# Kernel optimization log

Measured on AMD Instinct MI355X. Metric: run time of the kernel, lower is better.

The kernel has to match this reference:

```python
import jax, jax.numpy as jnp
import numpy as np

NT = 100000   # total word nodes (B graphs * N nodes)
B = 50        # number of graphs in the batch
E = 1600000   # total edges
V = 15000     # vocab (num_word)
D_IN = 128    # h_inp
D_H = 128     # h_dim


def setup_inputs() -> dict:
    key = jax.random.key(0)
    ks = jax.random.split(key, 12)
    return {
        "node_ids": jax.random.randint(ks[0], (NT,), 0, V),
        "src": jax.random.randint(ks[1], (E,), 0, NT),
        "dst": jax.random.randint(ks[2], (E,), 0, NT),
        "edge_weight": jax.random.uniform(ks[3], (E,), dtype=jnp.float32),
        "y_data": jax.random.uniform(ks[4], (B,), dtype=jnp.float32),
        "word_embeds": jax.random.normal(ks[5], (V, D_IN), dtype=jnp.float32) * 0.1,
        "W1": jax.random.normal(ks[6], (D_IN, D_H), dtype=jnp.float32) * 0.05,
        "b1": jax.random.normal(ks[7], (D_H,), dtype=jnp.float32) * 0.05,
        "W2": jax.random.normal(ks[8], (D_H, D_H), dtype=jnp.float32) * 0.05,
        "b2": jax.random.normal(ks[9], (D_H,), dtype=jnp.float32) * 0.05,
        "W_out": jax.random.normal(ks[10], (D_H, 1), dtype=jnp.float32) * 0.05,
        "b_out": jax.random.normal(ks[11], (1,), dtype=jnp.float32) * 0.05,
    }


def _word_graph_layer(h, W, b, src, dst, edge_weight, deg):
    # Linear projection, then DGL u_mul_e + mean aggregation over incoming edges.
    Wh = h @ W + b                                   # [NT, D]
    m = Wh[src] * edge_weight[:, None]               # gather + edge-weight mul, [E, D]
    s = jax.ops.segment_sum(m, dst, num_segments=NT)  # scatter-add, [NT, D]
    # mean over incoming messages; nodes with no in-edges keep 0 (DGL semantics)
    return jnp.where(deg[:, None] > 0, s / jnp.maximum(deg, 1.0)[:, None], 0.0)


def reference(node_ids, src, dst, edge_weight, y_data, word_embeds,
              W1, b1, W2, b2, W_out, b_out):
    deg = jax.ops.segment_sum(jnp.ones_like(edge_weight), dst, num_segments=NT)
    h = word_embeds[node_ids]                        # [NT, D_IN]
    h = _word_graph_layer(h, W1, b1, src, dst, edge_weight, deg)
    h = jax.nn.leaky_relu(h, negative_slope=0.01)
    h = _word_graph_layer(h, W2, b2, src, dst, edge_weight, deg)
    # per-graph mean pool; equal graph sizes so padded mean == true mean
    word_pool = h.reshape(B, NT // B, D_H).mean(axis=1)   # [B, D_H]
    logits = (word_pool @ W_out + b_out).reshape(-1)      # [B]
    # binary_cross_entropy_with_logits, mean reduction (numerically stable)
    loss = jnp.mean(jnp.maximum(logits, 0.0) - logits * y_data
                    + jnp.log1p(jnp.exp(-jnp.abs(logits))))
    y_pred = jax.nn.sigmoid(logits)[:, None]              # [B, 1]
    return (loss, y_pred)
```

## Files before the change

### kernel.cpp

```cpp
#include <hip/hip_runtime.h>
#include <hip/hip_fp16.h>
#include <math.h>

#define NT 100000
#define B_GRAPHS 50
#define NE 1600000
#define V 15000
#define D 128
#define NODES_PER_GRAPH (NT / B_GRAPHS)

#define POOL_N (B_GRAPHS * D + B_GRAPHS)

#define BSH 8
#define BIN_DSTS 256
#define NBIN ((NT + BIN_DSTS - 1) / BIN_DSTS)
#define SLACK (3 * BIN_DSTS)
#define EPB 4096
#define NFB ((NE + EPB - 1) / EPB)
#define BUF_SORT 5632
#define PAY_CAP2 (NE + NBIN * SLACK + 256)

__device__ __forceinline__ unsigned enc2_e5m2(float a, float b) {
  unsigned ha = __half_as_ushort(__float2half(a));
  unsigned hb = __half_as_ushort(__float2half(b));
  ha = ((ha + 0x7fu + ((ha >> 8) & 1u)) >> 8) & 0xffu;
  hb = ((hb + 0x7fu + ((hb >> 8) & 1u)) >> 8) & 0xffu;
  return ha | (hb << 8);
}
__device__ __forceinline__ unsigned enc4_e5m2(float a, float b, float c, float d) {
  return enc2_e5m2(a, b) | (enc2_e5m2(c, d) << 16);
}
__device__ __forceinline__ float4 dec4_e5m2(unsigned u) {
  unsigned hp0 = ((u & 0xffu) << 8) | ((u & 0xff00u) << 16);
  unsigned hp1 = ((u >> 8) & 0xff00u) | (u & 0xff000000u);
  __half2 h0 = *(__half2*)&hp0;
  __half2 h1 = *(__half2*)&hp1;
  float2 f0 = __half22float2(h0);
  float2 f1 = __half22float2(h1);
  return make_float4(f0.x, f0.y, f1.x, f1.y);
}

#define PR 16
__global__ __launch_bounds__(256, 8)
void k_project(const float* __restrict__ embeds,
               const float* __restrict__ W1,
               const float* __restrict__ b1,
               unsigned* __restrict__ P1p8) {
  __shared__ float sE[PR][D];
  __shared__ float sO[PR][D];
  int t = threadIdx.x;
  int row0 = blockIdx.x * PR;
  for (int i = t; i < PR * D; i += 256) {
    int r = i >> 7, c = i & 127;
    int v = row0 + r;
    sE[r][c] = (v < V) ? embeds[(size_t)v * D + c] : 0.f;
  }
  __syncthreads();
  int c = t & 127, rg = (t >> 7) * 8;
  float bd = b1[c];
  float acc[8];
#pragma unroll
  for (int r = 0; r < 8; ++r) acc[r] = bd;
#pragma unroll 4
  for (int k = 0; k < D; ++k) {
    float w = W1[k * D + c];
#pragma unroll
    for (int r = 0; r < 8; ++r) acc[r] = fmaf(sE[rg + r][k], w, acc[r]);
  }
#pragma unroll
  for (int r = 0; r < 8; ++r) sO[rg + r][c] = acc[r];
  __syncthreads();
  for (int i = t; i < PR * 32; i += 256) {
    int r = i >> 5, li = i & 31;
    int v = row0 + r;
    if (v < V)
      P1p8[(size_t)v * 32 + li] =
          enc4_e5m2(sO[r][4 * li], sO[r][4 * li + 1], sO[r][4 * li + 2], sO[r][4 * li + 3]);
  }
}

__global__ __launch_bounds__(512)
void k_hist(const int* __restrict__ dst, int* __restrict__ binCnt) {
  __shared__ int h[NBIN];
  int t = threadIdx.x;
  for (int i = t; i < NBIN; i += 512) h[i] = 0;
  __syncthreads();
  int base = blockIdx.x * EPB;
#pragma unroll
  for (int i = 0; i < EPB / 512; ++i) {
    int e = base + i * 512 + t;
    if (e < NE) atomicAdd(&h[dst[e] >> BSH], 1);
  }
  __syncthreads();
  for (int i = t; i < NBIN; i += 512)
    if (h[i]) atomicAdd(&binCnt[i], h[i]);
}

__global__ void k_binscan(const int* __restrict__ binCnt,
                          int* __restrict__ stageBase, int* __restrict__ payBase) {
  __shared__ int s[512], p[512];
  int t = threadIdx.x;
  int c = (t < NBIN) ? binCnt[t] : 0;
  int cp = (t < NBIN) ? (c + SLACK) : 0;
  s[t] = c; p[t] = cp;
  __syncthreads();
  for (int off = 1; off < 512; off <<= 1) {
    int a = (t >= off) ? s[t - off] : 0;
    int b = (t >= off) ? p[t - off] : 0;
    __syncthreads();
    s[t] += a; p[t] += b;
    __syncthreads();
  }
  if (t < NBIN) { stageBase[t] = s[t] - c; payBase[t] = p[t] - cp; }
}

__global__ __launch_bounds__(512)
void k_binfill(const int* __restrict__ src, const int* __restrict__ dst,
               const float* __restrict__ ew, const int* __restrict__ node_ids,
               const int* __restrict__ stageBase, int* __restrict__ binCursor,
               int2* __restrict__ stage) {
  __shared__ int h[512], sc[512], gbase[512], cur[512];
  __shared__ int2 buf[EPB];
  int t = threadIdx.x;
  h[t] = 0;
  __syncthreads();
  int base = blockIdx.x * EPB;
  int d_[EPB / 512], b_[EPB / 512];
#pragma unroll
  for (int i = 0; i < EPB / 512; ++i) {
    int e = base + i * 512 + t;
    int d = (e < NE) ? dst[e] : -1;
    d_[i] = d;
    b_[i] = (d >= 0) ? (d >> BSH) : -1;
    if (d >= 0) atomicAdd(&h[b_[i]], 1);
  }
  __syncthreads();
  int c = h[t];
  sc[t] = c;
  __syncthreads();
  for (int off = 1; off < 512; off <<= 1) {
    int a = (t >= off) ? sc[t - off] : 0;
    __syncthreads();
    sc[t] += a;
    __syncthreads();
  }
  cur[t] = sc[t] - c;
  if (t < NBIN && c > 0) gbase[t] = atomicAdd(&binCursor[t], c);
  __syncthreads();
#pragma unroll
  for (int i = 0; i < EPB / 512; ++i) {
    int e = base + i * 512 + t;
    if (e < NE) {
      int s = src[e];
      unsigned uw = __float_as_uint(ew[e]);
      unsigned wb = (uw + 0x7fffu + ((uw >> 16) & 1u)) & 0xffff0000u;
      int wid = node_ids[s];
      int dl = d_[i] & (BIN_DSTS - 1);
      int p = atomicAdd(&cur[b_[i]], 1);
      buf[p] = make_int2((int)(wb | (unsigned)wid), s | (dl << 17));
    }
  }
  __syncthreads();
  for (int b = t; b < NBIN; b += 512) {
    int len = h[b];
    if (!len) continue;
    int gp = stageBase[b] + gbase[b];
    int lp = sc[b] - len;
    for (int k = 0; k < len; ++k) stage[gp + k] = buf[lp + k];
  }
}

__global__ __launch_bounds__(256)
void k_binsort(const int2* __restrict__ stage, const int* __restrict__ binCnt,
               const int* __restrict__ stageBase, const int* __restrict__ payBase,
               int* __restrict__ rowD, int* __restrict__ cntD,
               int2* __restrict__ pay) {
  __shared__ int h2[BIN_DSTS], ro[BIN_DSTS], cur2[BIN_DSTS];
  __shared__ int2 buf[BUF_SORT];
  int b = blockIdx.x, t = threadIdx.x;
  int cnt = binCnt[b], sb = stageBase[b], pb = payBase[b];
  int dst0 = b << BSH;
  h2[t] = 0;
  __syncthreads();
  for (int i = t; i < cnt; i += 256)
    atomicAdd(&h2[(stage[sb + i].y >> 17) & 255], 1);
  __syncthreads();
  int c = h2[t];
  int pc = (c + 3) & ~3;
  ro[t] = pc;
  __syncthreads();
  for (int off = 1; off < 256; off <<= 1) {
    int a = (t >= off) ? ro[t - off] : 0;
    __syncthreads();
    ro[t] += a;
    __syncthreads();
  }
  int myoff = ro[t] - pc;
  int n = dst0 + t;
  if (n < NT) { rowD[n] = pb + myoff; cntD[n] = c; }
  cur2[t] = myoff;
  __syncthreads();
  int ztot = cnt + SLACK;
  for (int i = t; i < ztot; i += 256) buf[i] = make_int2(0, 0);
  __syncthreads();
  for (int i = t; i < cnt; i += 256) {
    int2 r = stage[sb + i];
    int dl = (r.y >> 17) & 255;
    int p = atomicAdd(&cur2[dl], 1);
    buf[p] = make_int2(r.x, r.y & 0x1ffff);
  }
  __syncthreads();
  for (int i = t; i < ztot; i += 256) pay[pb + i] = buf[i];
}

template<bool USE_WID>
__device__ __forceinline__ int pick_idx(const int4& q, int half) {
  int lo = USE_WID ? (q.x & 0xffff) : q.y;
  int hi = USE_WID ? (q.z & 0xffff) : q.w;
  return half ? hi : lo;
}
__device__ __forceinline__ void consume2(const int4& q, unsigned v, int half,
                                         float& a0, float& a1, float& a2, float& a3,
                                         float& sw) {
  int wm = half ? q.z : q.x;
  float w = __uint_as_float((unsigned)wm & 0xffff0000u);
  float4 x = dec4_e5m2(v);
  a0 = fmaf(w, x.x, a0); a1 = fmaf(w, x.y, a1);
  a2 = fmaf(w, x.z, a2); a3 = fmaf(w, x.w, a3);
  sw += w;
}

template<bool USE_WID>
__device__ __forceinline__ void gather_row(const int2* __restrict__ pay,
                                           const unsigned* __restrict__ tab,
                                           int beg, int cnt, int li, int half,
                                           float& a0, float& a1, float& a2, float& a3,
                                           float& sw) {
  int G = (cnt + 3) >> 2;
  const int4* __restrict__ pp = (const int4*)(pay + beg);
  int4 q0a = pp[0], q0b = pp[1];
  int4 q1a = pp[2], q1b = pp[3];
  int4 q2a = pp[4], q2b = pp[5];
  int4 q3a = pp[6], q3b = pp[7];
  int4 q4a = pp[8], q4b = pp[9];
  unsigned va0 = tab[(size_t)pick_idx<USE_WID>(q0a, half) * 32 + li];
  unsigned vb0 = tab[(size_t)pick_idx<USE_WID>(q0b, half) * 32 + li];
  unsigned va1 = tab[(size_t)pick_idx<USE_WID>(q1a, half) * 32 + li];
  unsigned vb1 = tab[(size_t)pick_idx<USE_WID>(q1b, half) * 32 + li];
  unsigned va2 = tab[(size_t)pick_idx<USE_WID>(q2a, half) * 32 + li];
  unsigned vb2 = tab[(size_t)pick_idx<USE_WID>(q2b, half) * 32 + li];
  for (int g = 0; g < G; ++g) {
    unsigned vn0 = tab[(size_t)pick_idx<USE_WID>(q3a, half) * 32 + li];
    unsigned vn1 = tab[(size_t)pick_idx<USE_WID>(q3b, half) * 32 + li];
    int4 qna = pp[2 * g + 10];
    int4 qnb = pp[2 * g + 11];
    consume2(q0a, va0, half, a0, a1, a2, a3, sw);
    consume2(q0b, vb0, half, a0, a1, a2, a3, sw);
    q0a = q1a; q0b = q1b; q1a = q2a; q1b = q2b; q2a = q3a; q2b = q3b;
    q3a = q4a; q3b = q4b; q4a = qna; q4b = qnb;
    va0 = va1; vb0 = vb1; va1 = va2; vb1 = vb2; va2 = vn0; vb2 = vn1;
  }
}

__global__ void k_agg1(const int2* __restrict__ pay,
                       const int* __restrict__ rowD, const int* __restrict__ cntD,
                       const unsigned* __restrict__ P1p8,
                       unsigned* __restrict__ h1p8) {
  int n = blockIdx.x * 4 + (threadIdx.x >> 6);
  int lane = threadIdx.x & 63;
  int li = lane & 31, half = lane >> 5;
  int beg = __builtin_amdgcn_readfirstlane(rowD[n]);
  int cnt = __builtin_amdgcn_readfirstlane(cntD[n]);
  float a0 = 0.f, a1 = 0.f, a2 = 0.f, a3 = 0.f, sw = 0.f;
  gather_row<true>(pay, P1p8, beg, cnt, li, half, a0, a1, a2, a3, sw);
  a0 += __shfl_down(a0, 32);
  a1 += __shfl_down(a1, 32);
  a2 += __shfl_down(a2, 32);
  a3 += __shfl_down(a3, 32);
  if (lane < 32) {
    float inv = (cnt > 0) ? (1.0f / (float)cnt) : 0.0f;
    float x0 = a0 * inv, x1 = a1 * inv, x2 = a2 * inv, x3 = a3 * inv;
    x0 = (x0 > 0.f) ? x0 : 0.01f * x0;
    x1 = (x1 > 0.f) ? x1 : 0.01f * x1;
    x2 = (x2 > 0.f) ? x2 : 0.01f * x2;
    x3 = (x3 > 0.f) ? x3 : 0.01f * x3;
    h1p8[(size_t)n * 32 + li] = enc4_e5m2(x0, x1, x2, x3);
  }
}

#define NPW2 10
#define BLKS_PER_G (NODES_PER_GRAPH / (4 * NPW2))
__global__ void k_agg2(const int2* __restrict__ pay,
                       const int* __restrict__ rowD, const int* __restrict__ cntD,
                       const unsigned* __restrict__ h1p8,
                       float* __restrict__ pool) {
  int g = blockIdx.x / BLKS_PER_G;
  int chunk = blockIdx.x % BLKS_PER_G;
  int w = threadIdx.x >> 6, lane = threadIdx.x & 63;
  int li = lane & 31, half = lane >> 5;
  int nbase = g * NODES_PER_GRAPH + chunk * (4 * NPW2) + w * NPW2;
  float s0 = 0.f, s1 = 0.f, s2 = 0.f, s3 = 0.f, sc = 0.f;
  for (int i = 0; i < NPW2; ++i) {
    int n = nbase + i;
    int beg = __builtin_amdgcn_readfirstlane(rowD[n]);
    int cnt = __builtin_amdgcn_readfirstlane(cntD[n]);
    float a0 = 0.f, a1 = 0.f, a2 = 0.f, a3 = 0.f, sw = 0.f;
    gather_row<false>(pay, h1p8, beg, cnt, li, half, a0, a1, a2, a3, sw);
    float inv = (cnt > 0) ? (1.0f / (float)cnt) : 0.0f;
    s0 = fmaf(a0, inv, s0); s1 = fmaf(a1, inv, s1);
    s2 = fmaf(a2, inv, s2); s3 = fmaf(a3, inv, s3);
    sc = fmaf(sw, inv, sc);
  }
  s0 += __shfl_down(s0, 32);
  s1 += __shfl_down(s1, 32);
  s2 += __shfl_down(s2, 32);
  s3 += __shfl_down(s3, 32);
  sc += __shfl_down(sc, 32);
  __shared__ float sS[4 * 128];
  __shared__ float sC[4];
  if (lane < 32) {
    sS[w * 128 + 4 * li + 0] = s0;
    sS[w * 128 + 4 * li + 1] = s1;
    sS[w * 128 + 4 * li + 2] = s2;
    sS[w * 128 + 4 * li + 3] = s3;
  }
  if (lane == 0) sC[w] = sc;
  __syncthreads();
  int t = threadIdx.x;
  if (t < 128) {
    float v = sS[t] + sS[128 + t] + sS[256 + t] + sS[384 + t];
    atomicAdd(&pool[g * D + t], v);
  }
  if (t == 0) atomicAdd(&pool[B_GRAPHS * D + g], sC[0] + sC[1] + sC[2] + sC[3]);
}

__global__ void k_final(const float* __restrict__ poolS, const float* __restrict__ poolC,
                        const float* __restrict__ W2, const float* __restrict__ b2,
                        const float* __restrict__ W_out, const float* __restrict__ b_out,
                        const float* __restrict__ y, float* __restrict__ out) {
  int t = threadIdx.x;
  __shared__ float w2o[D];
  __shared__ float red[D];
  __shared__ float s2o_sh;
  __shared__ float logits[B_GRAPHS];
  float acc = 0.f;
  for (int d = 0; d < D; ++d) acc = fmaf(W2[t * D + d], W_out[d], acc);
  w2o[t] = acc;
  red[t] = b2[t] * W_out[t];
  __syncthreads();
  for (int off = 64; off > 0; off >>= 1) {
    if (t < off) red[t] += red[t + off];
    __syncthreads();
  }
  if (t == 0) s2o_sh = red[0];
  __syncthreads();
  float s2o = s2o_sh;
  float bout = b_out[0];
  const float invN = 1.0f / (float)NODES_PER_GRAPH;
  for (int g = 0; g < B_GRAPHS; ++g) {
    red[t] = poolS[g * D + t] * w2o[t];
    __syncthreads();
    for (int off = 64; off > 0; off >>= 1) {
      if (t < off) red[t] += red[t + off];
      __syncthreads();
    }
    if (t == 0) logits[g] = red[0] * invN + poolC[g] * invN * s2o + bout;
    __syncthreads();
  }
  float term = 0.f;
  if (t < B_GRAPHS) {
    float l = logits[t];
    out[1 + t] = 1.0f / (1.0f + expf(-l));
    term = fmaxf(l, 0.f) - l * y[t] + log1pf(expf(-fabsf(l)));
  }
  red[t] = term;
  __syncthreads();
  for (int off = 64; off > 0; off >>= 1) {
    if (t < off) red[t] += red[t + off];
    __syncthreads();
  }
  if (t == 0) out[0] = red[0] / (float)B_GRAPHS;
}

extern "C" void kernel_launch(void* const* d_in, const int* in_sizes, int n_in,
                              void* d_out, int out_size, void* d_ws, size_t ws_size,
                              hipStream_t stream) {
  const int*   node_ids = (const int*)d_in[0];
  const int*   src      = (const int*)d_in[1];
  const int*   dst      = (const int*)d_in[2];
  const float* ew       = (const float*)d_in[3];
  const float* y        = (const float*)d_in[4];
  const float* embeds   = (const float*)d_in[5];
  const float* W1       = (const float*)d_in[6];
  const float* b1       = (const float*)d_in[7];
  const float* W2       = (const float*)d_in[8];
  const float* b2       = (const float*)d_in[9];
  const float* W_out    = (const float*)d_in[10];
  const float* b_out    = (const float*)d_in[11];
  float* out = (float*)d_out;
  (void)in_sizes; (void)n_in; (void)out_size; (void)ws_size;

  char* ws = (char*)d_ws;
  size_t off = 0;
  auto alloc = [&](size_t bytes) {
    size_t r = off;
    off = (off + bytes + 511) & ~(size_t)511;
    return r;
  };
  size_t o_binCnt = alloc(512 * 4);
  size_t o_binCur = alloc(512 * 4);
  size_t o_pool   = alloc((size_t)POOL_N * 4);
  size_t zero_end = off;
  size_t o_sBase  = alloc(512 * 4);
  size_t o_pBase  = alloc(512 * 4);
  size_t o_rowD   = alloc((size_t)NT * 4);
  size_t o_cntD   = alloc((size_t)NT * 4);
  size_t o_P1p8   = alloc((size_t)V * 32 * 4);
  size_t o_h1p8   = alloc((size_t)NT * 32 * 4);
  size_t o_stage  = alloc((size_t)NE * 8);
  size_t o_pay    = alloc((size_t)PAY_CAP2 * 8);

  int*      binCnt   = (int*)(ws + o_binCnt);
  int*      binCursor= (int*)(ws + o_binCur);
  float*    pool     = (float*)(ws + o_pool);
  int*      stageBase= (int*)(ws + o_sBase);
  int*      payBase  = (int*)(ws + o_pBase);
  int*      rowD     = (int*)(ws + o_rowD);
  int*      cntD     = (int*)(ws + o_cntD);
  unsigned* P1p8     = (unsigned*)(ws + o_P1p8);
  unsigned* h1p8     = (unsigned*)(ws + o_h1p8);
  int2*     stage    = (int2*)(ws + o_stage);
  int2*     pay      = (int2*)(ws + o_pay);

  hipMemsetAsync(ws, 0, zero_end, stream);
  hipMemsetAsync(pay + (PAY_CAP2 - 256), 0, 256 * 8, stream);

  k_project<<<(V + PR - 1) / PR, 256, 0, stream>>>(embeds, W1, b1, P1p8);
  k_hist<<<NFB, 512, 0, stream>>>(dst, binCnt);
  k_binscan<<<1, 512, 0, stream>>>(binCnt, stageBase, payBase);
  k_binfill<<<NFB, 512, 0, stream>>>(src, dst, ew, node_ids,
                                     stageBase, binCursor, stage);
  k_binsort<<<NBIN, 256, 0, stream>>>(stage, binCnt, stageBase, payBase,
                                      rowD, cntD, pay);
  k_agg1<<<NT / 4, 256, 0, stream>>>(pay, rowD, cntD, P1p8, h1p8);
  k_agg2<<<B_GRAPHS * BLKS_PER_G, 256, 0, stream>>>(pay, rowD, cntD, h1p8, pool);
  k_final<<<1, 128, 0, stream>>>(pool, pool + B_GRAPHS * D, W2, b2, W_out, b_out, y, out);
}
```

Baseline: 303.3 us.

## Fold mean-degree scaling into edge weights and flatten layer-2 edge loop per graph

The binsort kernel now premultiplies each edge weight by 1/in-degree of its destination and rounds the product back to bf16. Layer 1 therefore drops its per-node scaling, and layer 2 can treat a graph's edges as one flat stream. Each wave of k_agg2 takes an even share of the graph's padded edge groups instead of walking 10 nodes with uneven degree, which balances load and cuts per-node loop overhead. It relies on zero-weight padding slots being harmless and on pay regions being contiguous per graph, and it adds one extra bf16 rounding of the scaled weight.

```diff
diff --git a/kernel.cpp b/kernel.cpp
--- a/kernel.cpp
+++ b/kernel.cpp
@@ -18,7 +18,9 @@
 #define EPB 4096
 #define NFB ((NE + EPB - 1) / EPB)
 #define BUF_SORT 5632
-#define PAY_CAP2 (NE + NBIN * SLACK + 256)
+#define PAY_CAP2 (NE + NBIN * (SLACK + 4) + 512)
+
+#define A2_BPG 32
 
 __device__ __forceinline__ unsigned enc2_e5m2(float a, float b) {
   unsigned ha = __half_as_ushort(__float2half(a));
@@ -97,11 +99,12 @@
 }
 
 __global__ void k_binscan(const int* __restrict__ binCnt,
-                          int* __restrict__ stageBase, int* __restrict__ payBase) {
+                          int* __restrict__ stageBase, int* __restrict__ payBase,
+                          int* __restrict__ rowD) {
   __shared__ int s[512], p[512];
   int t = threadIdx.x;
   int c = (t < NBIN) ? binCnt[t] : 0;
-  int cp = (t < NBIN) ? (c + SLACK) : 0;
+  int cp = (t < NBIN) ? ((c + SLACK + 3) & ~3) : 0;
   s[t] = c; p[t] = cp;
   __syncthreads();
   for (int off = 1; off < 512; off <<= 1) {
@@ -112,6 +115,7 @@
     __syncthreads();
   }
   if (t < NBIN) { stageBase[t] = s[t] - c; payBase[t] = p[t] - cp; }
+  if (t == NBIN - 1) rowD[NT] = p[t];
 }
 
 __global__ __launch_bounds__(512)
@@ -176,6 +180,7 @@
                int* __restrict__ rowD, int* __restrict__ cntD,
                int2* __restrict__ pay) {
   __shared__ int h2[BIN_DSTS], ro[BIN_DSTS], cur2[BIN_DSTS];
+  __shared__ float invD[BIN_DSTS];
   __shared__ int2 buf[BUF_SORT];
   int b = blockIdx.x, t = threadIdx.x;
   int cnt = binCnt[b], sb = stageBase[b], pb = payBase[b];
@@ -186,6 +191,7 @@
     atomicAdd(&h2[(stage[sb + i].y >> 17) & 255], 1);
   __syncthreads();
   int c = h2[t];
+  invD[t] = (c > 0) ? (1.0f / (float)c) : 0.0f;
   int pc = (c + 3) & ~3;
   ro[t] = pc;
   __syncthreads();
@@ -200,17 +206,21 @@
   if (n < NT) { rowD[n] = pb + myoff; cntD[n] = c; }
   cur2[t] = myoff;
   __syncthreads();
-  int ztot = cnt + SLACK;
-  for (int i = t; i < ztot; i += 256) buf[i] = make_int2(0, 0);
+  int cpL = (cnt + SLACK + 3) & ~3;
+  for (int i = t; i < cpL; i += 256) buf[i] = make_int2(0, 0);
   __syncthreads();
   for (int i = t; i < cnt; i += 256) {
     int2 r = stage[sb + i];
     int dl = (r.y >> 17) & 255;
+    float w = __uint_as_float((unsigned)r.x & 0xffff0000u);
+    float wp = w * invD[dl];
+    unsigned uw = __float_as_uint(wp);
+    unsigned wb2 = (uw + 0x7fffu + ((uw >> 16) & 1u)) & 0xffff0000u;
     int p = atomicAdd(&cur2[dl], 1);
-    buf[p] = make_int2(r.x, r.y & 0x1ffff);
-  }
-  __syncthreads();
-  for (int i = t; i < ztot; i += 256) pay[pb + i] = buf[i];
+    buf[p] = make_int2((int)(wb2 | ((unsigned)r.x & 0xffffu)), r.y & 0x1ffff);
+  }
+  __syncthreads();
+  for (int i = t; i < cpL; i += 256) pay[pb + i] = buf[i];
 }
 
 template<bool USE_WID>
@@ -278,8 +288,7 @@
   a2 += __shfl_down(a2, 32);
   a3 += __shfl_down(a3, 32);
   if (lane < 32) {
-    float inv = (cnt > 0) ? (1.0f / (float)cnt) : 0.0f;
-    float x0 = a0 * inv, x1 = a1 * inv, x2 = a2 * inv, x3 = a3 * inv;
+    float x0 = a0, x1 = a1, x2 = a2, x3 = a3;
     x0 = (x0 > 0.f) ? x0 : 0.01f * x0;
     x1 = (x1 > 0.f) ? x1 : 0.01f * x1;
     x2 = (x2 > 0.f) ? x2 : 0.01f * x2;
@@ -288,29 +297,25 @@
   }
 }
 
-#define NPW2 10
-#define BLKS_PER_G (NODES_PER_GRAPH / (4 * NPW2))
 __global__ void k_agg2(const int2* __restrict__ pay,
-                       const int* __restrict__ rowD, const int* __restrict__ cntD,
+                       const int* __restrict__ rowD,
                        const unsigned* __restrict__ h1p8,
                        float* __restrict__ pool) {
-  int g = blockIdx.x / BLKS_PER_G;
-  int chunk = blockIdx.x % BLKS_PER_G;
+  int g = blockIdx.x >> 5;
+  int blk = blockIdx.x & (A2_BPG - 1);
   int w = threadIdx.x >> 6, lane = threadIdx.x & 63;
   int li = lane & 31, half = lane >> 5;
-  int nbase = g * NODES_PER_GRAPH + chunk * (4 * NPW2) + w * NPW2;
+  int base = __builtin_amdgcn_readfirstlane(rowD[g * NODES_PER_GRAPH]);
+  int end  = __builtin_amdgcn_readfirstlane(
+      (g == B_GRAPHS - 1) ? rowD[NT] : rowD[(g + 1) * NODES_PER_GRAPH]);
+  int groups = (end - base) >> 2;
+  int gpw = (groups + 4 * A2_BPG - 1) / (4 * A2_BPG);
+  int slot = blk * 4 + w;
+  int g0 = slot * gpw;
+  int myg = groups - g0;
+  myg = (myg < 0) ? 0 : ((myg > gpw) ? gpw : myg);
   float s0 = 0.f, s1 = 0.f, s2 = 0.f, s3 = 0.f, sc = 0.f;
-  for (int i = 0; i < NPW2; ++i) {
-    int n = nbase + i;
-    int beg = __builtin_amdgcn_readfirstlane(rowD[n]);
-    int cnt = __builtin_amdgcn_readfirstlane(cntD[n]);
-    float a0 = 0.f, a1 = 0.f, a2 = 0.f, a3 = 0.f, sw = 0.f;
-    gather_row<false>(pay, h1p8, beg, cnt, li, half, a0, a1, a2, a3, sw);
-    float inv = (cnt > 0) ? (1.0f / (float)cnt) : 0.0f;
-    s0 = fmaf(a0, inv, s0); s1 = fmaf(a1, inv, s1);
-    s2 = fmaf(a2, inv, s2); s3 = fmaf(a3, inv, s3);
-    sc = fmaf(sw, inv, sc);
-  }
+  gather_row<false>(pay, h1p8, base + g0 * 4, myg * 4, li, half, s0, s1, s2, s3, sc);
   s0 += __shfl_down(s0, 32);
   s1 += __shfl_down(s1, 32);
   s2 += __shfl_down(s2, 32);
@@ -413,7 +418,7 @@
   size_t zero_end = off;
   size_t o_sBase  = alloc(512 * 4);
   size_t o_pBase  = alloc(512 * 4);
-  size_t o_rowD   = alloc((size_t)NT * 4);
+  size_t o_rowD   = alloc((size_t)(NT + 1) * 4);
   size_t o_cntD   = alloc((size_t)NT * 4);
   size_t o_P1p8   = alloc((size_t)V * 32 * 4);
   size_t o_h1p8   = alloc((size_t)NT * 32 * 4);
@@ -433,16 +438,16 @@
   int2*     pay      = (int2*)(ws + o_pay);
 
   hipMemsetAsync(ws, 0, zero_end, stream);
-  hipMemsetAsync(pay + (PAY_CAP2 - 256), 0, 256 * 8, stream);
+  hipMemsetAsync(pay + (PAY_CAP2 - 512), 0, 512 * 8, stream);
 
   k_project<<<(V + PR - 1) / PR, 256, 0, stream>>>(embeds, W1, b1, P1p8);
   k_hist<<<NFB, 512, 0, stream>>>(dst, binCnt);
-  k_binscan<<<1, 512, 0, stream>>>(binCnt, stageBase, payBase);
+  k_binscan<<<1, 512, 0, stream>>>(binCnt, stageBase, payBase, rowD);
   k_binfill<<<NFB, 512, 0, stream>>>(src, dst, ew, node_ids,
                                      stageBase, binCursor, stage);
   k_binsort<<<NBIN, 256, 0, stream>>>(stage, binCnt, stageBase, payBase,
                                       rowD, cntD, pay);
   k_agg1<<<NT / 4, 256, 0, stream>>>(pay, rowD, cntD, P1p8, h1p8);
-  k_agg2<<<B_GRAPHS * BLKS_PER_G, 256, 0, stream>>>(pay, rowD, cntD, h1p8, pool);
+  k_agg2<<<B_GRAPHS * A2_BPG, 256, 0, stream>>>(pay, rowD, h1p8, pool);
   k_final<<<1, 128, 0, stream>>>(pool, pool + B_GRAPHS * D, W2, b2, W_out, b_out, y, out);
 }
```

Result: slower. 311.0 us (+2.5%).
